# Kernel tuning notes

Measured on AMD Instinct MI355X. Metric: run time of the kernel, lower is better.

The kernel has to match this reference:

```python
import jax, jax.numpy as jnp
import numpy as np

N = 20000          # num nodes
DEG = 8            # directed avg degree before symmetrization
IN_C, HID, OUT_C, K = 128, 32, 16, 2


def _build_graph(n, deg, seed=0):
    """Build symmetric 1-hop A1 (no self loops) and exact 2-hop A2 edge lists,
    with D^{-1/2} A D^{-1/2} normalized values (mirrors _prepare_prop)."""
    rng = np.random.default_rng(seed)
    e = n * deg
    row = rng.integers(0, n, e)
    col = rng.integers(0, n, e)
    r = np.concatenate([row, col])
    c = np.concatenate([col, row])
    m = r != c
    keys1 = np.unique(r[m].astype(np.int64) * n + c[m])  # A1 = indicator(A - I)
    r1 = (keys1 // n).astype(np.int64)
    c1 = (keys1 % n).astype(np.int64)
    # exact 2-hop: nonzeros of A1@A1, minus A1 and diagonal
    degs = np.bincount(r1, minlength=n)
    indptr = np.concatenate([np.zeros(1, np.int64), np.cumsum(degs)])
    counts = degs[c1]                       # per edge (u,v): deg(v)
    cum = np.cumsum(counts)
    total = int(cum[-1])
    offs = np.arange(total) - np.repeat(cum - counts, counts)
    dst2 = c1[np.repeat(indptr[c1], counts) + offs]
    src2 = np.repeat(r1, counts)
    keys2 = np.unique(src2 * n + dst2)
    diag = np.arange(n, dtype=np.int64) * (n + 1)
    keys2 = np.setdiff1d(keys2, np.concatenate([keys1, diag]), assume_unique=True)
    r2 = (keys2 // n).astype(np.int64)
    c2 = (keys2 % n).astype(np.int64)

    def norm(rr, cc):  # D^{-1/2} A D^{-1/2} on binary symmetric adjacency
        d = np.bincount(rr, minlength=n).astype(np.float64)
        dis = np.where(d > 0, 1.0 / np.sqrt(np.maximum(d, 1.0)), 0.0)
        return (dis[rr] * dis[cc]).astype(np.float32)

    return r1, c1, norm(r1, c1), r2, c2, norm(r2, c2)


def setup_inputs() -> dict:
    key = jax.random.key(0)
    k1, k2, k3 = jax.random.split(key, 3)
    x = jax.random.normal(k1, (N, IN_C), dtype=jnp.float32)
    # xavier_uniform for the two dense weights
    ae = float(np.sqrt(6.0 / (IN_C + HID)))
    cdim = (2 ** (K + 1) - 1) * HID  # 224
    ac = float(np.sqrt(6.0 / (cdim + OUT_C)))
    w_embed = jax.random.uniform(k2, (IN_C, HID), jnp.float32, -ae, ae)
    w_classify = jax.random.uniform(k3, (cdim, OUT_C), jnp.float32, -ac, ac)
    r1, c1, v1, r2, c2, v2 = _build_graph(N, DEG)
    return {
        "x": x, "w_embed": w_embed, "w_classify": w_classify,
        "a1_row": jnp.asarray(r1), "a1_col": jnp.asarray(c1), "a1_val": jnp.asarray(v1),
        "a2_row": jnp.asarray(r2), "a2_col": jnp.asarray(c2), "a2_val": jnp.asarray(v2),
    }


def _spmm(row, col, val, x, n):
    # sparse @ dense: gather source rows, scale, scatter-add into dest rows
    return jax.ops.segment_sum(x[col] * val[:, None], row, num_segments=n)


def reference(x, w_embed, w_classify, a1_row, a1_col, a1_val, a2_row, a2_col, a2_val):
    n = x.shape[0]
    rs = [jax.nn.relu(x @ w_embed)]  # [N, HID]
    for _ in range(K):
        r = rs[-1]
        r1 = _spmm(a1_row, a1_col, a1_val, r, n)
        r2 = _spmm(a2_row, a2_col, a2_val, r, n)
        rs.append(jax.nn.relu(jnp.concatenate([r1, r2], axis=1)))
    r_final = jnp.concatenate(rs, axis=1)  # [N, 7*HID]; dropout is identity in eval
    return r_final @ w_classify            # [N, OUT_C]
```

## Files before the change

kernel.cpp:

```cpp
#include <hip/hip_runtime.h>

typedef unsigned int uint;
typedef unsigned short ushort;

#define IN_C 128
#define HID  32

__device__ __forceinline__ float bf_lo(uint u) { return __uint_as_float(u << 16); }
__device__ __forceinline__ float bf_hi(uint u) { return __uint_as_float(u & 0xffff0000u); }
__device__ __forceinline__ uint  f2bf(float f) {
    uint u = __float_as_uint(f);
    return (u + 0x7fffu + ((u >> 16) & 1u)) >> 16;
}

__global__ void prep_kernel(const float* __restrict__ x,
                            const float* __restrict__ w,
                            ushort* __restrict__ r0,
                            const int* __restrict__ a1r, int E1, int* __restrict__ ip1,
                            const int* __restrict__ a2r, int E2, int* __restrict__ ip2,
                            int n, int nbE) {
    __shared__ float wl[IN_C * HID];
    const int tid = threadIdx.x;
    if (blockIdx.x < nbE) {
        for (int i = tid; i < IN_C * HID; i += blockDim.x) wl[i] = w[i];
        __syncthreads();
        const int row = blockIdx.x * 16 + tid / 16;
        const int h0  = (tid % 16) * 2;
        if (row >= n) return;
        const float4* xr = (const float4*)(x + (size_t)row * IN_C);
        float a0 = 0.f, a1 = 0.f;
#pragma unroll
        for (int k4 = 0; k4 < IN_C / 4; ++k4) {
            float4 xv = xr[k4];
            a0 += xv.x * wl[(4*k4+0)*HID + h0];  a1 += xv.x * wl[(4*k4+0)*HID + h0+1];
            a0 += xv.y * wl[(4*k4+1)*HID + h0];  a1 += xv.y * wl[(4*k4+1)*HID + h0+1];
            a0 += xv.z * wl[(4*k4+2)*HID + h0];  a1 += xv.z * wl[(4*k4+2)*HID + h0+1];
            a0 += xv.w * wl[(4*k4+3)*HID + h0];  a1 += xv.w * wl[(4*k4+3)*HID + h0+1];
        }
        uint p = f2bf(fmaxf(a0, 0.f)) | (f2bf(fmaxf(a1, 0.f)) << 16);
        ((uint*)r0)[(size_t)row * 16 + (tid % 16)] = p;
    } else {
        const int i = (blockIdx.x - nbE) * 256 + tid;
        if (i > n) return;
        int lo = 0, hi = E1;
        while (lo < hi) { int m = (lo + hi) >> 1; if (a1r[m] < i) lo = m + 1; else hi = m; }
        ip1[i] = lo;
        lo = 0; hi = E2;
        while (lo < hi) { int m = (lo + hi) >> 1; if (a2r[m] < i) lo = m + 1; else hi = m; }
        ip2[i] = lo;
    }
}

template <int C, int ROWS>
__global__ __launch_bounds__(256) void spmm_level(
        const int* __restrict__ ip1, const int* __restrict__ col1,
        const float* __restrict__ val1,
        const int* __restrict__ ip2, const int* __restrict__ col2,
        const float* __restrict__ val2,
        const ushort* __restrict__ xin, ushort* __restrict__ out,
        int n, int nb2) {
    constexpr int L    = C / 8;
    constexpr int SUBL = 64 / ROWS;
    constexpr int W    = SUBL / L;
    const int lane = threadIdx.x & 63;
    const int wave = threadIdx.x >> 6;
    const int sub  = lane / SUBL;
    const int li   = lane % SUBL;
    const int fl   = li % L;
    const int way  = li / L;

    int bid = blockIdx.x;
    const int* ip; const int* col; const float* val; int off;
    if (bid < nb2) {             ip = ip2; col = col2; val = val2; off = C; }
    else           { bid -= nb2; ip = ip1; col = col1; val = val1; off = 0; }

    const int row = (bid * 4 + wave) * ROWS + sub;
    if (row >= n) return;

    const ushort* xbase = xin + fl * 8;
    float acc[8];
#pragma unroll
    for (int j = 0; j < 8; ++j) acc[j] = 0.f;

    auto gat = [&](int c) -> uint4 {
        return *(const uint4*)(xbase + (size_t)c * C);
    };
    auto fmadd = [&](const uint4& u, float v) {
        acc[0] += v * bf_lo(u.x); acc[1] += v * bf_hi(u.x);
        acc[2] += v * bf_lo(u.y); acc[3] += v * bf_hi(u.y);
        acc[4] += v * bf_lo(u.z); acc[5] += v * bf_hi(u.z);
        acc[6] += v * bf_lo(u.w); acc[7] += v * bf_hi(u.w);
    };

    const int s = ip[row];
    const int e = ip[row + 1];
    int sv = (s + 3) & ~3; if (sv > e) sv = e;
    for (int idx = s + way; idx < sv; idx += W) fmadd(gat(col[idx]), val[idx]);

    const int*   cb = col + sv;
    const float* vb = val + sv;
    const int nv8 = (e - sv) / (8 * W);
    for (int i = 0; i < nv8; ++i) {
        const int base = (i * W + way) * 8;
        const int4   c0 = *(const int4*)  (cb + base);
        const int4   c1 = *(const int4*)  (cb + base + 4);
        const float4 v0 = *(const float4*)(vb + base);
        const float4 v1 = *(const float4*)(vb + base + 4);
        const uint4 g0 = gat(c0.x), g1 = gat(c0.y), g2 = gat(c0.z), g3 = gat(c0.w);
        const uint4 g4 = gat(c1.x), g5 = gat(c1.y), g6 = gat(c1.z), g7 = gat(c1.w);
        fmadd(g0, v0.x); fmadd(g1, v0.y); fmadd(g2, v0.z); fmadd(g3, v0.w);
        fmadd(g4, v1.x); fmadd(g5, v1.y); fmadd(g6, v1.z); fmadd(g7, v1.w);
    }
    int done = sv + nv8 * 8 * W;
    const int nv4 = (e - done) / (4 * W);
    if (nv4 > 0) {
        const int base = (done - sv) + way * 4;
        const int4   c0 = *(const int4*)  (cb + base);
        const float4 v0 = *(const float4*)(vb + base);
        const uint4 g0 = gat(c0.x), g1 = gat(c0.y), g2 = gat(c0.z), g3 = gat(c0.w);
        fmadd(g0, v0.x); fmadd(g1, v0.y); fmadd(g2, v0.z); fmadd(g3, v0.w);
        done += 4 * W;
    }
    for (int idx = done + way; idx < e; idx += W) fmadd(gat(col[idx]), val[idx]);

#pragma unroll
    for (int m = L; m < SUBL; m <<= 1)
#pragma unroll
        for (int j = 0; j < 8; ++j) acc[j] += __shfl_xor(acc[j], m, 64);

    if (way == 0) {
        uint4 p;
        p.x = f2bf(fmaxf(acc[0],0.f)) | (f2bf(fmaxf(acc[1],0.f)) << 16);
        p.y = f2bf(fmaxf(acc[2],0.f)) | (f2bf(fmaxf(acc[3],0.f)) << 16);
        p.z = f2bf(fmaxf(acc[4],0.f)) | (f2bf(fmaxf(acc[5],0.f)) << 16);
        p.w = f2bf(fmaxf(acc[6],0.f)) | (f2bf(fmaxf(acc[7],0.f)) << 16);
        *(uint4*)(out + (size_t)row * (2 * C) + off + fl * 8) = p;
    }
}

#define CDIM 224
#define OUT_C 16
__global__ void classify_kernel(const ushort* __restrict__ r0,
                                const ushort* __restrict__ r1,
                                const ushort* __restrict__ r2,
                                const float* __restrict__ w,
                                float* __restrict__ out, int n) {
    __shared__ float wl[CDIM * OUT_C];
    const int tid = threadIdx.x;
    for (int i = tid; i < CDIM * OUT_C; i += blockDim.x) wl[i] = w[i];
    __syncthreads();
    const int row = blockIdx.x * 16 + tid / 16;
    const int o   = tid % 16;
    if (row >= n) return;
    float acc = 0.f;

    const uint4* a = (const uint4*)(r0 + (size_t)row * 32);
#pragma unroll
    for (int q = 0; q < 4; ++q) {
        uint4 u = a[q]; int j = q * 8;
        acc += bf_lo(u.x) * wl[(j+0)*OUT_C + o];  acc += bf_hi(u.x) * wl[(j+1)*OUT_C + o];
        acc += bf_lo(u.y) * wl[(j+2)*OUT_C + o];  acc += bf_hi(u.y) * wl[(j+3)*OUT_C + o];
        acc += bf_lo(u.z) * wl[(j+4)*OUT_C + o];  acc += bf_hi(u.z) * wl[(j+5)*OUT_C + o];
        acc += bf_lo(u.w) * wl[(j+6)*OUT_C + o];  acc += bf_hi(u.w) * wl[(j+7)*OUT_C + o];
    }
    const uint4* b = (const uint4*)(r1 + (size_t)row * 64);
#pragma unroll
    for (int q = 0; q < 8; ++q) {
        uint4 u = b[q]; int j = 32 + q * 8;
        acc += bf_lo(u.x) * wl[(j+0)*OUT_C + o];  acc += bf_hi(u.x) * wl[(j+1)*OUT_C + o];
        acc += bf_lo(u.y) * wl[(j+2)*OUT_C + o];  acc += bf_hi(u.y) * wl[(j+3)*OUT_C + o];
        acc += bf_lo(u.z) * wl[(j+4)*OUT_C + o];  acc += bf_hi(u.z) * wl[(j+5)*OUT_C + o];
        acc += bf_lo(u.w) * wl[(j+6)*OUT_C + o];  acc += bf_hi(u.w) * wl[(j+7)*OUT_C + o];
    }
    const uint4* c = (const uint4*)(r2 + (size_t)row * 128);
#pragma unroll
    for (int q = 0; q < 16; ++q) {
        uint4 u = c[q]; int j = 96 + q * 8;
        acc += bf_lo(u.x) * wl[(j+0)*OUT_C + o];  acc += bf_hi(u.x) * wl[(j+1)*OUT_C + o];
        acc += bf_lo(u.y) * wl[(j+2)*OUT_C + o];  acc += bf_hi(u.y) * wl[(j+3)*OUT_C + o];
        acc += bf_lo(u.z) * wl[(j+4)*OUT_C + o];  acc += bf_hi(u.z) * wl[(j+5)*OUT_C + o];
        acc += bf_lo(u.w) * wl[(j+6)*OUT_C + o];  acc += bf_hi(u.w) * wl[(j+7)*OUT_C + o];
    }
    out[(size_t)row * OUT_C + o] = acc;
}

extern "C" void kernel_launch(void* const* d_in, const int* in_sizes, int n_in,
                              void* d_out, int out_size, void* d_ws, size_t ws_size,
                              hipStream_t stream) {
    const float* x   = (const float*)d_in[0];
    const float* we  = (const float*)d_in[1];
    const float* wc  = (const float*)d_in[2];
    const int*   a1r = (const int*)  d_in[3];
    const int*   a1c = (const int*)  d_in[4];
    const float* a1v = (const float*)d_in[5];
    const int*   a2r = (const int*)  d_in[6];
    const int*   a2c = (const int*)  d_in[7];
    const float* a2v = (const float*)d_in[8];
    float* out = (float*)d_out;

    const int E1 = in_sizes[3];
    const int E2 = in_sizes[6];
    const int n  = in_sizes[0] / IN_C;

    ushort* r0 = (ushort*)d_ws;
    ushort* r1 = r0 + (size_t)n * 32;
    ushort* r2 = r1 + (size_t)n * 64;
    int*   ip1 = (int*)(r2 + (size_t)n * 128);
    int*   ip2 = ip1 + (n + 1);

    {
        const int nbE = (n + 15) / 16;
        const int nbI = (n + 1 + 255) / 256;
        prep_kernel<<<nbE + nbI, 256, 0, stream>>>(x, we, r0, a1r, E1, ip1,
                                                   a2r, E2, ip2, n, nbE);
    }

    {
        const int nb = (n + 7) / 8;
        spmm_level<32, 2><<<2 * nb, 256, 0, stream>>>(ip1, a1c, a1v, ip2, a2c, a2v,
                                                      r0, r1, n, nb);
    }
    {
        const int nb = (n + 3) / 4;
        spmm_level<64, 1><<<2 * nb, 256, 0, stream>>>(ip1, a1c, a1v, ip2, a2c, a2v,
                                                      r1, r2, n, nb);
    }

    classify_kernel<<<(n + 15) / 16, 256, 0, stream>>>(r0, r1, r2, wc, out, n);
}
```

Baseline: 237.5 us.

## Prefetch 2-hop edge arrays into cache during prep; simplify SpMM unrolled loop

```diff
diff --git a/kernel.cpp b/kernel.cpp
--- a/kernel.cpp
+++ b/kernel.cpp
@@ -18,7 +18,9 @@
                             ushort* __restrict__ r0,
                             const int* __restrict__ a1r, int E1, int* __restrict__ ip1,
                             const int* __restrict__ a2r, int E2, int* __restrict__ ip2,
-                            int n, int nbE) {
+                            const int* __restrict__ a2c, const float* __restrict__ a2v,
+                            float* __restrict__ dummy,
+                            int n, int nbE, int nbI, int nbT) {
     __shared__ float wl[IN_C * HID];
     const int tid = threadIdx.x;
     if (blockIdx.x < nbE) {
@@ -39,7 +41,7 @@
         }
         uint p = f2bf(fmaxf(a0, 0.f)) | (f2bf(fmaxf(a1, 0.f)) << 16);
         ((uint*)r0)[(size_t)row * 16 + (tid % 16)] = p;
-    } else {
+    } else if (blockIdx.x < nbE + nbI) {
         const int i = (blockIdx.x - nbE) * 256 + tid;
         if (i > n) return;
         int lo = 0, hi = E1;
@@ -48,6 +50,18 @@
         lo = 0; hi = E2;
         while (lo < hi) { int m = (lo + hi) >> 1; if (a2r[m] < i) lo = m + 1; else hi = m; }
         ip2[i] = lo;
+    } else {
+        const int t = (blockIdx.x - nbE - nbI) * 256 + tid;
+        const int stride = nbT * 256;
+        const int total4 = E2 / 4;
+        const float4* c4 = (const float4*)a2c;
+        const float4* v4 = (const float4*)a2v;
+        float s = 0.f;
+        for (int i = t; i < total4; i += stride) {
+            float4 u = c4[i], v = v4[i];
+            s += u.x + u.y + u.z + u.w + v.x + v.y + v.z + v.w;
+        }
+        if (s == 123.456f) dummy[0] = s;
     }
 }
 
@@ -95,33 +109,21 @@
     const int s = ip[row];
     const int e = ip[row + 1];
     int sv = (s + 3) & ~3; if (sv > e) sv = e;
+    const int nv = (e - sv) / (4 * W);
+
     for (int idx = s + way; idx < sv; idx += W) fmadd(gat(col[idx]), val[idx]);
 
     const int*   cb = col + sv;
     const float* vb = val + sv;
-    const int nv8 = (e - sv) / (8 * W);
-    for (int i = 0; i < nv8; ++i) {
-        const int base = (i * W + way) * 8;
-        const int4   c0 = *(const int4*)  (cb + base);
-        const int4   c1 = *(const int4*)  (cb + base + 4);
-        const float4 v0 = *(const float4*)(vb + base);
-        const float4 v1 = *(const float4*)(vb + base + 4);
-        const uint4 g0 = gat(c0.x), g1 = gat(c0.y), g2 = gat(c0.z), g3 = gat(c0.w);
-        const uint4 g4 = gat(c1.x), g5 = gat(c1.y), g6 = gat(c1.z), g7 = gat(c1.w);
-        fmadd(g0, v0.x); fmadd(g1, v0.y); fmadd(g2, v0.z); fmadd(g3, v0.w);
-        fmadd(g4, v1.x); fmadd(g5, v1.y); fmadd(g6, v1.z); fmadd(g7, v1.w);
-    }
-    int done = sv + nv8 * 8 * W;
-    const int nv4 = (e - done) / (4 * W);
-    if (nv4 > 0) {
-        const int base = (done - sv) + way * 4;
-        const int4   c0 = *(const int4*)  (cb + base);
-        const float4 v0 = *(const float4*)(vb + base);
-        const uint4 g0 = gat(c0.x), g1 = gat(c0.y), g2 = gat(c0.z), g3 = gat(c0.w);
-        fmadd(g0, v0.x); fmadd(g1, v0.y); fmadd(g2, v0.z); fmadd(g3, v0.w);
-        done += 4 * W;
-    }
-    for (int idx = done + way; idx < e; idx += W) fmadd(gat(col[idx]), val[idx]);
+    for (int i = 0; i < nv; ++i) {
+        const int base = (i * W + way) * 4;
+        const int4   cc = *(const int4*)  (cb + base);
+        const float4 vv = *(const float4*)(vb + base);
+        const uint4 g0 = gat(cc.x), g1 = gat(cc.y), g2 = gat(cc.z), g3 = gat(cc.w);
+        fmadd(g0, vv.x); fmadd(g1, vv.y); fmadd(g2, vv.z); fmadd(g3, vv.w);
+    }
+    for (int idx = sv + nv * 4 * W + way; idx < e; idx += W)
+        fmadd(gat(col[idx]), val[idx]);
 
 #pragma unroll
     for (int m = L; m < SUBL; m <<= 1)
@@ -207,12 +209,15 @@
     ushort* r2 = r1 + (size_t)n * 64;
     int*   ip1 = (int*)(r2 + (size_t)n * 128);
     int*   ip2 = ip1 + (n + 1);
+    float* dummy = (float*)(ip2 + (n + 2));
 
     {
         const int nbE = (n + 15) / 16;
         const int nbI = (n + 1 + 255) / 256;
-        prep_kernel<<<nbE + nbI, 256, 0, stream>>>(x, we, r0, a1r, E1, ip1,
-                                                   a2r, E2, ip2, n, nbE);
+        const int nbT = 512;
+        prep_kernel<<<nbE + nbI + nbT, 256, 0, stream>>>(
+            x, we, r0, a1r, E1, ip1, a2r, E2, ip2, a2c, a2v, dummy,
+            n, nbE, nbI, nbT);
     }
 
     {
```

Result: faster. 217.6 us (-8.4%).
